# Optimization experiments

Measured on AMD Instinct MI355X. Metric: run time of the kernel, lower is better.

The kernel has to match this reference:

```python
import jax, jax.numpy as jnp
import numpy as np
from jax import lax

N = 16384          # num_nodes (LSTM sequence length, batch=1)
AVG_DEG = 32
E_EDGES = N * AVG_DEG
FEAT = 512         # cmd_args.feat_dim (tag vocab)
EMB = 256          # embedding_size -> LSTM input = 2*EMB
H = 512            # LSTM hidden_size
MLP_H = 512        # cmd_args.hidden
C = 10             # cmd_args.num_class


def setup_inputs() -> dict:
    key = jax.random.key(0)
    ks = jax.random.split(key, 14)
    s = 1.0 / np.sqrt(H)
    u = lambda k, shape: jax.random.uniform(k, shape, jnp.float32, -s, s)
    return {
        "node_tags": jax.random.randint(ks[0], (N,), 0, FEAT),
        "neighbor_node_ids": jax.random.randint(ks[1], (E_EDGES,), 0, N),
        "neighbor_tag_ids": jax.random.randint(ks[2], (E_EDGES,), 0, FEAT),
        "label": jax.random.randint(ks[3], (1,), 0, C),
        "W_emb": u(ks[4], (FEAT, EMB)),
        "b_emb": u(ks[5], (EMB,)),
        "W_ih": u(ks[6], (4 * H, 2 * EMB)),  # torch LSTM gate order: i, f, g, o
        "W_hh": u(ks[7], (4 * H, H)),
        "b_lstm": u(ks[8], (4 * H,)),        # b_ih + b_hh folded together
        "W1": u(ks[9], (H, MLP_H)),
        "b1": u(ks[10], (MLP_H,)),
        "W2": u(ks[11], (MLP_H, C)),
        "b2": u(ks[12], (C,)),
    }


def reference(node_tags, neighbor_node_ids, neighbor_tag_ids, label,
              W_emb, b_emb, W_ih, W_hh, b_lstm, W1, b1, W2, b2):
    n = node_tags.shape[0]
    feat_dim = W_emb.shape[0]
    hid = W_hh.shape[1]

    # one-hot(node_tags) @ W_emb + b  ==  row-gather of W_emb
    node_emb = W_emb[node_tags] + b_emb                      # [N, EMB]

    # ragged neighbor-tag histogram via scatter-add (the Python double loop)
    hist = jnp.zeros((n, feat_dim), dtype=W_emb.dtype)
    hist = hist.at[neighbor_node_ids, neighbor_tag_ids].add(1.0)  # [N, FEAT]
    nb_emb = hist @ W_emb + b_emb                            # [N, EMB]

    x = jnp.concatenate([node_emb, nb_emb], axis=1)          # [N, 2*EMB]

    # single-layer LSTM, batch=1, seq_len=N; precompute input projections
    pre = x @ W_ih.T + b_lstm                                # [N, 4H]

    def step(carry, p):
        h, c = carry
        g = p + h @ W_hh.T                                   # [4H]
        i, f, gg, o = jnp.split(g, 4)
        i = jax.nn.sigmoid(i)
        f = jax.nn.sigmoid(f)
        o = jax.nn.sigmoid(o)
        c = f * c + i * jnp.tanh(gg)
        h = o * jnp.tanh(c)
        return (h, c), h

    init = (jnp.zeros((hid,), x.dtype), jnp.zeros((hid,), x.dtype))
    _, hs = lax.scan(step, init, pre)                        # hs: [N, H]

    embed = jnp.sum(hs, axis=0)[None, :]                     # [1, H] (sum over time)

    # MLPClassifier: Linear -> ReLU -> Linear -> log_softmax
    h1 = jax.nn.relu(embed @ W1 + b1)
    logits = h1 @ W2 + b2                                    # [1, C]
    return jax.nn.log_softmax(logits, axis=-1)
```

## Files before the change

### kernel.cpp

```cpp
#include <hip/hip_runtime.h>
#include <hip/hip_bf16.h>

#define N_NODES 16384
#define E_EDGESN (16384*32)
#define FEAT 512
#define EMB 256
#define HID 512
#define G4 2048
#define XDIM 512
#define NWG 16
#define UPW 32

typedef __attribute__((ext_vector_type(8))) short bf16x8;
typedef __attribute__((ext_vector_type(4))) float f32x4;

__device__ __forceinline__ float b2f(unsigned short u) {
  union { unsigned int i; float f; } v; v.i = ((unsigned int)u) << 16; return v.f;
}
__device__ __forceinline__ unsigned short f2b(float f) {
  union { float f; unsigned int i; } v; v.f = f;
  unsigned int x = v.i;
  unsigned int r = (x + 0x7FFFu + ((x >> 16) & 1u)) >> 16;
  return (unsigned short)r;
}
__device__ __forceinline__ float sigmoidf_(float x) { return 1.0f / (1.0f + __expf(-x)); }

__global__ __launch_bounds__(256) void k_detect(const unsigned* __restrict__ w,
                                                unsigned* __restrict__ flag) {
  __shared__ int cnt;
  if (threadIdx.x == 0) cnt = 0;
  __syncthreads();
  int hits = 0;
#pragma unroll
  for (int j = 0; j < 4; ++j) {
    unsigned wv = w[threadIdx.x * 4 + j];
    unsigned e = (wv >> 7) & 0xFFu;
    if ((e >= 90u && e <= 126u) || ((wv & 0xFFFFu) == 0u)) hits++;
  }
  atomicAdd(&cnt, hits);
  __syncthreads();
  if (threadIdx.x == 0) *flag = (cnt < 512) ? 1u : 0u;
}

__global__ void k_convert(const void* __restrict__ src, unsigned short* __restrict__ dst,
                          int n, const unsigned* __restrict__ flag) {
  int i = blockIdx.x * blockDim.x + threadIdx.x;
  if (i >= n) return;
  if (*flag) dst[i] = f2b(((const float*)src)[i]);
  else       dst[i] = ((const unsigned short*)src)[i];
}

__global__ void k_hist(const int* __restrict__ nid, const int* __restrict__ ntag,
                       unsigned* __restrict__ hist) {
  int e = blockIdx.x * blockDim.x + threadIdx.x;
  if (e < E_EDGESN)
    atomicAdd(&hist[(size_t)nid[e] * FEAT + ntag[e]], 1u);
}

__global__ __launch_bounds__(256) void k_build_x(
    const int* __restrict__ tags, const unsigned* __restrict__ hist,
    const unsigned short* __restrict__ Wemb, const unsigned short* __restrict__ bemb,
    unsigned short* __restrict__ x) {
  __shared__ int f_lds[160];
  __shared__ float c_lds[160];
  __shared__ int nlist;
  int n = blockIdx.x, c = threadIdx.x;
  if (c == 0) nlist = 0;
  __syncthreads();
  for (int f = c; f < FEAT; f += 256) {
    unsigned cnt = hist[(size_t)n * FEAT + f];
    if (cnt) {
      int idx = atomicAdd(&nlist, 1);
      if (idx < 160) { f_lds[idx] = f; c_lds[idx] = (float)cnt; }
    }
  }
  __syncthreads();
  int m = nlist; if (m > 160) m = 160;
  float be = b2f(bemb[c]);
  int tg = tags[n];
  x[(size_t)n * XDIM + c] = f2b(b2f(Wemb[(size_t)tg * EMB + c]) + be);
  float acc = be;
  for (int j = 0; j < m; ++j)
    acc += c_lds[j] * b2f(Wemb[(size_t)f_lds[j] * EMB + c]);
  x[(size_t)n * XDIM + EMB + c] = f2b(acc);
}

__global__ __launch_bounds__(256) void k_gemm_pre(
    const unsigned short* __restrict__ x, const unsigned short* __restrict__ Wih,
    const unsigned short* __restrict__ blstm, unsigned short* __restrict__ pre) {
  int wave = threadIdx.x >> 6, lane = threadIdx.x & 63;
  int row = lane & 15, quad = lane >> 4;
  int mband = blockIdx.y * 64 + wave * 16;
  int nbase = blockIdx.x * 128;
  f32x4 acc[8] = {};
  const unsigned short* ap = x + (size_t)(mband + row) * XDIM + quad * 8;
  const unsigned short* bp0 = Wih + (size_t)(nbase + row) * XDIM + quad * 8;
  for (int kc = 0; kc < 16; ++kc) {
    bf16x8 af = *(const bf16x8*)(ap + kc * 32);
#pragma unroll
    for (int nt = 0; nt < 8; ++nt) {
      bf16x8 bf = *(const bf16x8*)(bp0 + (size_t)nt * 16 * XDIM + kc * 32);
      acc[nt] = __builtin_amdgcn_mfma_f32_16x16x32_bf16(af, bf, acc[nt], 0, 0, 0);
    }
  }
#pragma unroll
  for (int nt = 0; nt < 8; ++nt) {
    int nn = nbase + nt * 16 + row;
    float bv = b2f(blstm[nn]);
#pragma unroll
    for (int i = 0; i < 4; ++i) {
      int mm = mband + quad * 4 + i;
      pre[(size_t)mm * G4 + nn] = f2b(acc[nt][i] + bv);
    }
  }
}

__global__ __launch_bounds__(512, 2) void k_scan(
    const unsigned short* __restrict__ Whh, const unsigned short* __restrict__ pre,
    unsigned* __restrict__ hw, float* __restrict__ embed) {
  __shared__ float h_lds[HID];
  __shared__ float g_lds[128];
  int tid = threadIdx.x, wg = blockIdx.x;
  int rg = tid >> 4, s = tid & 15;

  int growA[4];
  float wreg[4][32];
#pragma unroll
  for (int rr = 0; rr < 4; ++rr) {
    int r = rg * 4 + rr;
    int grow = (r >> 5) * HID + wg * UPW + (r & 31);
    growA[rr] = grow;
    const unsigned short* wp = Whh + (size_t)grow * HID;
#pragma unroll
    for (int j = 0; j < 16; ++j) {
      wreg[rr][2 * j]     = b2f(wp[32 * j + 2 * s]);
      wreg[rr][2 * j + 1] = b2f(wp[32 * j + 2 * s + 1]);
    }
  }

  float pcur[4];
#pragma unroll
  for (int rr = 0; rr < 4; ++rr) pcur[rr] = b2f(pre[growA[rr]]);

  h_lds[tid] = 0.0f;
  float cstate = 0.0f, eacc = 0.0f;
  __syncthreads();

  for (int t = 0; t < N_NODES; ++t) {
    float a0 = 0.f, a1 = 0.f, a2 = 0.f, a3 = 0.f;
    const float2* hb = (const float2*)h_lds;
#pragma unroll
    for (int j = 0; j < 16; ++j) {
      float2 hv = hb[j * 16 + s];
      a0 += wreg[0][2*j] * hv.x + wreg[0][2*j+1] * hv.y;
      a1 += wreg[1][2*j] * hv.x + wreg[1][2*j+1] * hv.y;
      a2 += wreg[2][2*j] * hv.x + wreg[2][2*j+1] * hv.y;
      a3 += wreg[3][2*j] * hv.x + wreg[3][2*j+1] * hv.y;
    }
#pragma unroll
    for (int off = 1; off < 16; off <<= 1) {
      a0 += __shfl_xor(a0, off);
      a1 += __shfl_xor(a1, off);
      a2 += __shfl_xor(a2, off);
      a3 += __shfl_xor(a3, off);
    }
    if (s == 0) {
      g_lds[rg * 4 + 0] = a0 + pcur[0];
      g_lds[rg * 4 + 1] = a1 + pcur[1];
      g_lds[rg * 4 + 2] = a2 + pcur[2];
      g_lds[rg * 4 + 3] = a3 + pcur[3];
    }
    __syncthreads();

    unsigned tagw = (unsigned)t & 0xFFFFu;
    unsigned base = ((unsigned)t & 1u) * 1024u;
    if (tid < UPW) {
      float gi = sigmoidf_(g_lds[tid]);
      float gf = sigmoidf_(g_lds[32 + tid]);
      float gg = tanhf(g_lds[64 + tid]);
      float go = sigmoidf_(g_lds[96 + tid]);
      cstate = gf * cstate + gi * gg;
      float hn = go * tanhf(cstate);
      eacc += hn;
      union { float f; unsigned u; } cu; cu.f = hn;
      __hip_atomic_store(&hw[base + wg * UPW + tid], (cu.u & 0xFFFF0000u) | tagw,
                         __ATOMIC_RELAXED, __HIP_MEMORY_SCOPE_AGENT);
      __hip_atomic_store(&hw[base + 512 + wg * UPW + tid], (cu.u << 16) | tagw,
                         __ATOMIC_RELAXED, __HIP_MEMORY_SCOPE_AGENT);
    }
    if (s == 0 && (t + 1) < N_NODES) {
#pragma unroll
      for (int rr = 0; rr < 4; ++rr)
        pcur[rr] = b2f(pre[(size_t)(t + 1) * G4 + growA[rr]]);
    }
    if (t < N_NODES - 1) {
      unsigned v0, v1;
      for (;;) {
        v0 = __hip_atomic_load(&hw[base + tid],       __ATOMIC_RELAXED, __HIP_MEMORY_SCOPE_AGENT);
        v1 = __hip_atomic_load(&hw[base + 512 + tid], __ATOMIC_RELAXED, __HIP_MEMORY_SCOPE_AGENT);
        if ((((v0 ^ tagw) | (v1 ^ tagw)) & 0xFFFFu) == 0u) break;
        __builtin_amdgcn_s_sleep(1);
      }
      union { unsigned u; float f; } rc; rc.u = (v0 & 0xFFFF0000u) | (v1 >> 16);
      h_lds[tid] = rc.f;
      __syncthreads();
    }
  }
  if (tid < UPW) embed[wg * UPW + tid] = eacc;
}

__global__ __launch_bounds__(512) void k_head(
    const float* __restrict__ embed, const unsigned short* __restrict__ W1,
    const unsigned short* __restrict__ b1, const unsigned short* __restrict__ W2,
    const unsigned short* __restrict__ b2, void* __restrict__ out,
    const unsigned* __restrict__ flag) {
  __shared__ float e_s[HID], h1_s[HID];
  __shared__ float lg[16];
  int tid = threadIdx.x;
  e_s[tid] = embed[tid];
  __syncthreads();
  float sum = b2f(b1[tid]);
  for (int i = 0; i < HID; ++i)
    sum += e_s[i] * b2f(W1[(size_t)i * HID + tid]);
  h1_s[tid] = fmaxf(sum, 0.0f);
  __syncthreads();
  if (tid < 10) {
    float l = b2f(b2[tid]);
    for (int j = 0; j < HID; ++j)
      l += h1_s[j] * b2f(W2[(size_t)j * 10 + tid]);
    lg[tid] = l;
  }
  __syncthreads();
  if (tid == 0) {
    float m = -1e30f;
    for (int c = 0; c < 10; ++c) m = fmaxf(m, lg[c]);
    float se = 0.f;
    for (int c = 0; c < 10; ++c) se += expf(lg[c] - m);
    float lse = m + logf(se);
    if (*flag) {
      for (int c = 0; c < 10; ++c) ((float*)out)[c] = lg[c] - lse;
    } else {
      for (int c = 0; c < 10; ++c) ((unsigned short*)out)[c] = f2b(lg[c] - lse);
    }
  }
}

extern "C" void kernel_launch(void* const* d_in, const int* in_sizes, int n_in,
                              void* d_out, int out_size, void* d_ws, size_t ws_size,
                              hipStream_t stream) {
  const int* node_tags = (const int*)d_in[0];
  const int* nid = (const int*)d_in[1];
  const int* ntag = (const int*)d_in[2];

  char* ws = (char*)d_ws;
  unsigned short* pre  = (unsigned short*)ws;
  unsigned short* x    = (unsigned short*)(ws + 67108864);
  unsigned*       hist = (unsigned*)(ws + 83886080);
  char* tail = ws + 117440512;
  unsigned* hw    = (unsigned*)tail;
  unsigned* flag  = (unsigned*)(tail + 8192);
  float*    embed = (float*)(tail + 8448);
  char* wc = ws + 117456896;
  unsigned short* Wemb_c  = (unsigned short*)(wc);
  unsigned short* bemb_c  = (unsigned short*)(wc + 262144);
  unsigned short* Wih_c   = (unsigned short*)(wc + 262656);
  unsigned short* Whh_c   = (unsigned short*)(wc + 2359808);
  unsigned short* blstm_c = (unsigned short*)(wc + 4456960);
  unsigned short* W1_c    = (unsigned short*)(wc + 4461056);
  unsigned short* b1_c    = (unsigned short*)(wc + 4985344);
  unsigned short* W2_c    = (unsigned short*)(wc + 4986368);
  unsigned short* b2_c    = (unsigned short*)(wc + 4996608);

  hipMemsetAsync(hist, 0, 33554432, stream);

  k_detect<<<1, 256, 0, stream>>>((const unsigned*)d_in[6], flag);

  struct { const void* s; unsigned short* d; int n; } cv[9] = {
    { d_in[4],  Wemb_c,  FEAT * EMB },
    { d_in[5],  bemb_c,  EMB },
    { d_in[6],  Wih_c,   G4 * XDIM },
    { d_in[7],  Whh_c,   G4 * HID },
    { d_in[8],  blstm_c, G4 },
    { d_in[9],  W1_c,    HID * HID },
    { d_in[10], b1_c,    HID },
    { d_in[11], W2_c,    HID * 10 },
    { d_in[12], b2_c,    10 },
  };
  for (int i = 0; i < 9; ++i)
    k_convert<<<(cv[i].n + 255) / 256, 256, 0, stream>>>(cv[i].s, cv[i].d, cv[i].n, flag);

  k_hist<<<E_EDGESN / 256, 256, 0, stream>>>(nid, ntag, hist);
  k_build_x<<<N_NODES, 256, 0, stream>>>(node_tags, hist, Wemb_c, bemb_c, x);
  k_gemm_pre<<<dim3(G4 / 128, N_NODES / 64), 256, 0, stream>>>(x, Wih_c, blstm_c, pre);
  k_scan<<<NWG, 512, 0, stream>>>(Whh_c, pre, hw, embed);
  k_head<<<1, 512, 0, stream>>>(embed, W1_c, b1_c, W2_c, b2_c, d_out, flag);
}
```

Before: 32.83 ms.

## Co-locate LSTM scan workgroups on one XCD and streamline per-step gate exchange

Launches extra scan workgroups and uses an atomic election on the hardware XCC ID so the 16 working groups all run on the same XCD, keeping the cross-workgroup hidden-state exchange within one L2. It reorders the precomputed gate layout so each hidden unit's four gates sit next to each other. This lets each 16-lane group finish its own cell update without the shared-memory gate step and its extra barrier. The h exchange uses 64-bit stores and polling loads with explicit cache bits, and the gate activations use rcp-based sigmoid and tanh approximations. The risks are slightly lower precision, reliance on the XCD hardware register and on enough workgroups landing on one XCD, and extra launched blocks that exit early.

Measured after the change: 33.33 ms. Within noise of the previous version (+1.5%).

```diff
diff --git a/kernel.cpp b/kernel.cpp
--- a/kernel.cpp
+++ b/kernel.cpp
@@ -9,6 +9,7 @@
 #define G4 2048
 #define XDIM 512
 #define NWG 16
+#define NLAUNCH 128
 #define UPW 32
 
 typedef __attribute__((ext_vector_type(8))) short bf16x8;
@@ -23,7 +24,12 @@
   unsigned int r = (x + 0x7FFFu + ((x >> 16) & 1u)) >> 16;
   return (unsigned short)r;
 }
-__device__ __forceinline__ float sigmoidf_(float x) { return 1.0f / (1.0f + __expf(-x)); }
+__device__ __forceinline__ float fast_sigmoid(float x) {
+  return __builtin_amdgcn_rcpf(1.0f + __expf(-x));
+}
+__device__ __forceinline__ float fast_tanh(float x) {
+  return fmaf(-2.0f, __builtin_amdgcn_rcpf(1.0f + __expf(2.0f * x)), 1.0f);
+}
 
 __global__ __launch_bounds__(256) void k_detect(const unsigned* __restrict__ w,
                                                 unsigned* __restrict__ flag) {
@@ -107,44 +113,64 @@
   for (int nt = 0; nt < 8; ++nt) {
     int nn = nbase + nt * 16 + row;
     float bv = b2f(blstm[nn]);
+    int pn = ((nn & 511) << 2) | (nn >> 9);
 #pragma unroll
     for (int i = 0; i < 4; ++i) {
       int mm = mband + quad * 4 + i;
-      pre[(size_t)mm * G4 + nn] = f2b(acc[nt][i] + bv);
+      pre[(size_t)mm * G4 + pn] = f2b(acc[nt][i] + bv);
     }
   }
 }
 
 __global__ __launch_bounds__(512, 2) void k_scan(
-    const unsigned short* __restrict__ Whh, const unsigned short* __restrict__ pre,
-    unsigned* __restrict__ hw, float* __restrict__ embed) {
+    const unsigned short* __restrict__ Whh, const unsigned short* __restrict__ prep,
+    unsigned* __restrict__ hw, float* __restrict__ embed, int* __restrict__ elect) {
   __shared__ float h_lds[HID];
-  __shared__ float g_lds[128];
-  int tid = threadIdx.x, wg = blockIdx.x;
-  int rg = tid >> 4, s = tid & 15;
-
-  int growA[4];
+  __shared__ int rank_s;
+  int tid = threadIdx.x;
+
+  if (tid == 0) {
+    unsigned xcd;
+    asm volatile("s_getreg_b32 %0, hwreg(HW_REG_XCC_ID)" : "=s"(xcd));
+    xcd &= 7u;
+    int idx = atomicAdd(&elect[xcd], 1);
+    int rank = -1;
+    if (idx < NWG) {
+      if (idx == NWG - 1) atomicCAS(&elect[8], -1, (int)xcd);
+      int w;
+      while ((w = __hip_atomic_load(&elect[8], __ATOMIC_RELAXED,
+                                    __HIP_MEMORY_SCOPE_AGENT)) == -1)
+        __builtin_amdgcn_s_sleep(8);
+      if (w == (int)xcd) rank = idx;
+    }
+    rank_s = rank;
+  }
+  __syncthreads();
+  int wg = rank_s;
+  if (wg < 0) return;
+
+  int ug = tid >> 4;
+  int s  = tid & 15;
+  int unit = wg * UPW + ug;
+
   float wreg[4][32];
 #pragma unroll
-  for (int rr = 0; rr < 4; ++rr) {
-    int r = rg * 4 + rr;
-    int grow = (r >> 5) * HID + wg * UPW + (r & 31);
-    growA[rr] = grow;
-    const unsigned short* wp = Whh + (size_t)grow * HID;
+  for (int g = 0; g < 4; ++g) {
+    const unsigned short* wp = Whh + (size_t)(g * HID + unit) * HID;
 #pragma unroll
     for (int j = 0; j < 16; ++j) {
-      wreg[rr][2 * j]     = b2f(wp[32 * j + 2 * s]);
-      wreg[rr][2 * j + 1] = b2f(wp[32 * j + 2 * s + 1]);
-    }
-  }
-
-  float pcur[4];
-#pragma unroll
-  for (int rr = 0; rr < 4; ++rr) pcur[rr] = b2f(pre[growA[rr]]);
-
+      wreg[g][2 * j]     = b2f(wp[32 * j + 2 * s]);
+      wreg[g][2 * j + 1] = b2f(wp[32 * j + 2 * s + 1]);
+    }
+  }
+
+  ushort4 pc = *(const ushort4*)(prep + (size_t)unit * 4);
+  float cstate = 0.0f, eacc = 0.0f;
   h_lds[tid] = 0.0f;
-  float cstate = 0.0f, eacc = 0.0f;
-  __syncthreads();
+  __syncthreads();
+
+  unsigned long long hwB = (unsigned long long)hw;
+  int pollslow = 0;
 
   for (int t = 0; t < N_NODES; ++t) {
     float a0 = 0.f, a1 = 0.f, a2 = 0.f, a3 = 0.f;
@@ -164,49 +190,57 @@
       a2 += __shfl_xor(a2, off);
       a3 += __shfl_xor(a3, off);
     }
+
+    unsigned tagw = (unsigned)t;
+    unsigned long long sbase = hwB + (unsigned)((t & 1) << 12);
+
     if (s == 0) {
-      g_lds[rg * 4 + 0] = a0 + pcur[0];
-      g_lds[rg * 4 + 1] = a1 + pcur[1];
-      g_lds[rg * 4 + 2] = a2 + pcur[2];
-      g_lds[rg * 4 + 3] = a3 + pcur[3];
-    }
-    __syncthreads();
-
-    unsigned tagw = (unsigned)t & 0xFFFFu;
-    unsigned base = ((unsigned)t & 1u) * 1024u;
-    if (tid < UPW) {
-      float gi = sigmoidf_(g_lds[tid]);
-      float gf = sigmoidf_(g_lds[32 + tid]);
-      float gg = tanhf(g_lds[64 + tid]);
-      float go = sigmoidf_(g_lds[96 + tid]);
+      float gi = fast_sigmoid(a0 + b2f(pc.x));
+      float gf = fast_sigmoid(a1 + b2f(pc.y));
+      float gg = fast_tanh   (a2 + b2f(pc.z));
+      float go = fast_sigmoid(a3 + b2f(pc.w));
       cstate = gf * cstate + gi * gg;
-      float hn = go * tanhf(cstate);
+      float hn = go * fast_tanh(cstate);
       eacc += hn;
-      union { float f; unsigned u; } cu; cu.f = hn;
-      __hip_atomic_store(&hw[base + wg * UPW + tid], (cu.u & 0xFFFF0000u) | tagw,
-                         __ATOMIC_RELAXED, __HIP_MEMORY_SCOPE_AGENT);
-      __hip_atomic_store(&hw[base + 512 + wg * UPW + tid], (cu.u << 16) | tagw,
-                         __ATOMIC_RELAXED, __HIP_MEMORY_SCOPE_AGENT);
-    }
-    if (s == 0 && (t + 1) < N_NODES) {
-#pragma unroll
-      for (int rr = 0; rr < 4; ++rr)
-        pcur[rr] = b2f(pre[(size_t)(t + 1) * G4 + growA[rr]]);
-    }
+      if (t < N_NODES - 1) {
+        union { float f; unsigned u; } cu; cu.f = hn;
+        unsigned long long sv =
+            ((unsigned long long)((cu.u << 16) | tagw) << 32) |
+            (unsigned long long)((cu.u & 0xFFFF0000u) | tagw);
+        unsigned long long sa = sbase + 8u * (unsigned)unit;
+        asm volatile("global_store_dwordx2 %0, %1, off sc0 sc1"
+                     :: "v"(sa), "v"(sv) : "memory");
+      }
+    }
+    if (s == 0 && (t + 1) < N_NODES)
+      pc = *(const ushort4*)(prep + (size_t)(t + 1) * G4 + unit * 4);
+
     if (t < N_NODES - 1) {
+      unsigned long long pa = sbase + 8u * (unsigned)tid;
+      unsigned long long v64;
       unsigned v0, v1;
+      int spins = 0;
       for (;;) {
-        v0 = __hip_atomic_load(&hw[base + tid],       __ATOMIC_RELAXED, __HIP_MEMORY_SCOPE_AGENT);
-        v1 = __hip_atomic_load(&hw[base + 512 + tid], __ATOMIC_RELAXED, __HIP_MEMORY_SCOPE_AGENT);
-        if ((((v0 ^ tagw) | (v1 ^ tagw)) & 0xFFFFu) == 0u) break;
-        __builtin_amdgcn_s_sleep(1);
+        if (!pollslow) {
+          asm volatile("global_load_dwordx2 %0, %1, off sc0\n\ts_waitcnt vmcnt(0)"
+                       : "=v"(v64) : "v"(pa) : "memory");
+          v0 = (unsigned)v64; v1 = (unsigned)(v64 >> 32);
+          if ((((v0 ^ tagw) | (v1 ^ tagw)) & 0xFFFFu) == 0u) break;
+          if (++spins > 4096) pollslow = 1;
+        } else {
+          unsigned* pp = (unsigned*)(uintptr_t)pa;
+          v0 = __hip_atomic_load(pp,     __ATOMIC_RELAXED, __HIP_MEMORY_SCOPE_AGENT);
+          v1 = __hip_atomic_load(pp + 1, __ATOMIC_RELAXED, __HIP_MEMORY_SCOPE_AGENT);
+          if ((((v0 ^ tagw) | (v1 ^ tagw)) & 0xFFFFu) == 0u) break;
+          __builtin_amdgcn_s_sleep(1);
+        }
       }
       union { unsigned u; float f; } rc; rc.u = (v0 & 0xFFFF0000u) | (v1 >> 16);
       h_lds[tid] = rc.f;
       __syncthreads();
     }
   }
-  if (tid < UPW) embed[wg * UPW + tid] = eacc;
+  if (s == 0) embed[unit] = eacc;
 }
 
 __global__ __launch_bounds__(512) void k_head(
@@ -260,6 +294,7 @@
   unsigned* hw    = (unsigned*)tail;
   unsigned* flag  = (unsigned*)(tail + 8192);
   float*    embed = (float*)(tail + 8448);
+  int*      elect = (int*)(tail + 10496);
   char* wc = ws + 117456896;
   unsigned short* Wemb_c  = (unsigned short*)(wc);
   unsigned short* bemb_c  = (unsigned short*)(wc + 262144);
@@ -272,6 +307,8 @@
   unsigned short* b2_c    = (unsigned short*)(wc + 4996608);
 
   hipMemsetAsync(hist, 0, 33554432, stream);
+  hipMemsetAsync(elect, 0, 32, stream);
+  hipMemsetAsync(elect + 8, 0xFF, 4, stream);
 
   k_detect<<<1, 256, 0, stream>>>((const unsigned*)d_in[6], flag);
 
@@ -292,6 +329,6 @@
   k_hist<<<E_EDGESN / 256, 256, 0, stream>>>(nid, ntag, hist);
   k_build_x<<<N_NODES, 256, 0, stream>>>(node_tags, hist, Wemb_c, bemb_c, x);
   k_gemm_pre<<<dim3(G4 / 128, N_NODES / 64), 256, 0, stream>>>(x, Wih_c, blstm_c, pre);
-  k_scan<<<NWG, 512, 0, stream>>>(Whh_c, pre, hw, embed);
+  k_scan<<<NLAUNCH, 512, 0, stream>>>(Whh_c, pre, hw, embed, elect);
   k_head<<<1, 512, 0, stream>>>(embed, W1_c, b1_c, W2_c, b2_c, d_out, flag);
 }
```

## Restructure LSTM scan: per-unit gate ownership, direct global h reads, interleaved pre layout

Applied to the files above, without the earlier changes.

The recurrent scan now runs across 32 workgroups of 256 threads. Each 16-lane group owns all four gates of one hidden unit, so there is no LDS gate exchange or block barrier. The hidden state is published as one tagged 32-bit word per unit, with an 8-bit step tag packed into the low mantissa bits. Each lane reads its slice of h directly from global memory with cache-bypassing batched loads and checks the tags, which replaces the LDS staging and __syncthreads. The pre-activation GEMM writes gates interleaved per unit, so each unit's four gates come from two dwords prefetched eight steps ahead. Sigmoid and tanh use rcp-based fast approximations. The cost is reduced h precision (24-bit float, 8-bit tag), a shorter tag that wraps sooner, and more polling traffic per lane.

New measurement: 86.79 ms. +164.3%, slower.

```diff
diff --git a/kernel.cpp b/kernel.cpp
--- a/kernel.cpp
+++ b/kernel.cpp
@@ -8,8 +8,8 @@
 #define HID 512
 #define G4 2048
 #define XDIM 512
-#define NWG 16
-#define UPW 32
+#define NWG 32
+#define UPW 16
 
 typedef __attribute__((ext_vector_type(8))) short bf16x8;
 typedef __attribute__((ext_vector_type(4))) float f32x4;
@@ -23,7 +23,12 @@
   unsigned int r = (x + 0x7FFFu + ((x >> 16) & 1u)) >> 16;
   return (unsigned short)r;
 }
-__device__ __forceinline__ float sigmoidf_(float x) { return 1.0f / (1.0f + __expf(-x)); }
+__device__ __forceinline__ float fast_sigmoid(float x) {
+  return __builtin_amdgcn_rcpf(1.0f + __expf(-x));
+}
+__device__ __forceinline__ float fast_tanh(float x) {
+  return fmaf(-2.0f, __builtin_amdgcn_rcpf(1.0f + __expf(2.0f * x)), 1.0f);
+}
 
 __global__ __launch_bounds__(256) void k_detect(const unsigned* __restrict__ w,
                                                 unsigned* __restrict__ flag) {
@@ -107,55 +112,124 @@
   for (int nt = 0; nt < 8; ++nt) {
     int nn = nbase + nt * 16 + row;
     float bv = b2f(blstm[nn]);
+    int pn = ((nn & 511) << 2) | (nn >> 9);
 #pragma unroll
     for (int i = 0; i < 4; ++i) {
       int mm = mband + quad * 4 + i;
-      pre[(size_t)mm * G4 + nn] = f2b(acc[nt][i] + bv);
-    }
-  }
-}
-
-__global__ __launch_bounds__(512, 2) void k_scan(
-    const unsigned short* __restrict__ Whh, const unsigned short* __restrict__ pre,
+      pre[(size_t)mm * G4 + pn] = f2b(acc[nt][i] + bv);
+    }
+  }
+}
+
+__global__ __launch_bounds__(256, 1) void k_scan(
+    const unsigned short* __restrict__ Whh, const unsigned short* __restrict__ prep,
     unsigned* __restrict__ hw, float* __restrict__ embed) {
-  __shared__ float h_lds[HID];
-  __shared__ float g_lds[128];
   int tid = threadIdx.x, wg = blockIdx.x;
-  int rg = tid >> 4, s = tid & 15;
-
-  int growA[4];
+  int ug = tid >> 4;
+  int s  = tid & 15;
+  int lane = tid & 63;
+  int unit = wg * UPW + ug;
+
   float wreg[4][32];
 #pragma unroll
-  for (int rr = 0; rr < 4; ++rr) {
-    int r = rg * 4 + rr;
-    int grow = (r >> 5) * HID + wg * UPW + (r & 31);
-    growA[rr] = grow;
-    const unsigned short* wp = Whh + (size_t)grow * HID;
+  for (int g = 0; g < 4; ++g) {
+    const unsigned* wp = (const unsigned*)(Whh + (size_t)(g * HID + unit) * HID) + s * 16;
 #pragma unroll
     for (int j = 0; j < 16; ++j) {
-      wreg[rr][2 * j]     = b2f(wp[32 * j + 2 * s]);
-      wreg[rr][2 * j + 1] = b2f(wp[32 * j + 2 * s + 1]);
-    }
-  }
-
-  float pcur[4];
-#pragma unroll
-  for (int rr = 0; rr < 4; ++rr) pcur[rr] = b2f(pre[growA[rr]]);
-
-  h_lds[tid] = 0.0f;
+      unsigned wv = wp[j];
+      wreg[g][2 * j]     = b2f((unsigned short)(wv & 0xFFFFu));
+      wreg[g][2 * j + 1] = b2f((unsigned short)(wv >> 16));
+    }
+  }
+
+  unsigned pc0[8], pc1[8];
+  if (s == 1) {
+#pragma unroll
+    for (int i = 0; i < 8; ++i) {
+      const unsigned* pp = (const unsigned*)(prep + (size_t)i * G4 + (unsigned)unit * 4u);
+      pc0[i] = pp[0]; pc1[i] = pp[1];
+    }
+  }
+  int bsrc = (lane & 48) | 1;
+
   float cstate = 0.0f, eacc = 0.0f;
-  __syncthreads();
+  unsigned long long hwB = (unsigned long long)hw;
+  unsigned w32[32];
+#pragma unroll
+  for (int i = 0; i < 32; ++i) w32[i] = 0;
 
   for (int t = 0; t < N_NODES; ++t) {
+    if (t > 0) {
+      unsigned tagp = (unsigned)(t - 1) & 0xFFu;
+      unsigned long long pa = hwB + (unsigned)(((t - 1) & 1) << 11) + (unsigned)s * 128u;
+      unsigned long long r0,r1,r2,r3,r4,r5,r6,r7,r8,r9,r10,r11,r12,r13,r14,r15;
+      int ok = 0;
+      for (int tries = 0; tries < 64 && !ok; ++tries) {
+        asm volatile(
+          "global_load_dwordx2 %0, %16, off sc0 sc1\n\t"
+          "global_load_dwordx2 %1, %16, off offset:8 sc0 sc1\n\t"
+          "global_load_dwordx2 %2, %16, off offset:16 sc0 sc1\n\t"
+          "global_load_dwordx2 %3, %16, off offset:24 sc0 sc1\n\t"
+          "global_load_dwordx2 %4, %16, off offset:32 sc0 sc1\n\t"
+          "global_load_dwordx2 %5, %16, off offset:40 sc0 sc1\n\t"
+          "global_load_dwordx2 %6, %16, off offset:48 sc0 sc1\n\t"
+          "global_load_dwordx2 %7, %16, off offset:56 sc0 sc1\n\t"
+          "global_load_dwordx2 %8, %16, off offset:64 sc0 sc1\n\t"
+          "global_load_dwordx2 %9, %16, off offset:72 sc0 sc1\n\t"
+          "global_load_dwordx2 %10, %16, off offset:80 sc0 sc1\n\t"
+          "global_load_dwordx2 %11, %16, off offset:88 sc0 sc1\n\t"
+          "global_load_dwordx2 %12, %16, off offset:96 sc0 sc1\n\t"
+          "global_load_dwordx2 %13, %16, off offset:104 sc0 sc1\n\t"
+          "global_load_dwordx2 %14, %16, off offset:112 sc0 sc1\n\t"
+          "global_load_dwordx2 %15, %16, off offset:120 sc0 sc1\n\t"
+          "s_waitcnt vmcnt(0)"
+          : "=&v"(r0), "=&v"(r1), "=&v"(r2), "=&v"(r3),
+            "=&v"(r4), "=&v"(r5), "=&v"(r6), "=&v"(r7),
+            "=&v"(r8), "=&v"(r9), "=&v"(r10), "=&v"(r11),
+            "=&v"(r12), "=&v"(r13), "=&v"(r14), "=&v"(r15)
+          : "v"(pa) : "memory");
+        w32[0]=(unsigned)r0;  w32[1]=(unsigned)(r0>>32);
+        w32[2]=(unsigned)r1;  w32[3]=(unsigned)(r1>>32);
+        w32[4]=(unsigned)r2;  w32[5]=(unsigned)(r2>>32);
+        w32[6]=(unsigned)r3;  w32[7]=(unsigned)(r3>>32);
+        w32[8]=(unsigned)r4;  w32[9]=(unsigned)(r4>>32);
+        w32[10]=(unsigned)r5; w32[11]=(unsigned)(r5>>32);
+        w32[12]=(unsigned)r6; w32[13]=(unsigned)(r6>>32);
+        w32[14]=(unsigned)r7; w32[15]=(unsigned)(r7>>32);
+        w32[16]=(unsigned)r8; w32[17]=(unsigned)(r8>>32);
+        w32[18]=(unsigned)r9; w32[19]=(unsigned)(r9>>32);
+        w32[20]=(unsigned)r10; w32[21]=(unsigned)(r10>>32);
+        w32[22]=(unsigned)r11; w32[23]=(unsigned)(r11>>32);
+        w32[24]=(unsigned)r12; w32[25]=(unsigned)(r12>>32);
+        w32[26]=(unsigned)r13; w32[27]=(unsigned)(r13>>32);
+        w32[28]=(unsigned)r14; w32[29]=(unsigned)(r14>>32);
+        w32[30]=(unsigned)r15; w32[31]=(unsigned)(r15>>32);
+        unsigned m = 0;
+#pragma unroll
+        for (int i = 0; i < 32; ++i) m |= (w32[i] ^ tagp);
+        ok = ((m & 0xFFu) == 0u);
+      }
+      if (!ok) {
+        unsigned* qp = (unsigned*)(uintptr_t)pa;
+#pragma unroll
+        for (int i = 0; i < 32; ++i) {
+          unsigned v;
+          do {
+            v = __hip_atomic_load(qp + i, __ATOMIC_RELAXED, __HIP_MEMORY_SCOPE_AGENT);
+          } while (((v ^ tagp) & 0xFFu) != 0u);
+          w32[i] = v;
+        }
+      }
+    }
+
     float a0 = 0.f, a1 = 0.f, a2 = 0.f, a3 = 0.f;
-    const float2* hb = (const float2*)h_lds;
-#pragma unroll
-    for (int j = 0; j < 16; ++j) {
-      float2 hv = hb[j * 16 + s];
-      a0 += wreg[0][2*j] * hv.x + wreg[0][2*j+1] * hv.y;
-      a1 += wreg[1][2*j] * hv.x + wreg[1][2*j+1] * hv.y;
-      a2 += wreg[2][2*j] * hv.x + wreg[2][2*j+1] * hv.y;
-      a3 += wreg[3][2*j] * hv.x + wreg[3][2*j+1] * hv.y;
+#pragma unroll
+    for (int j = 0; j < 32; ++j) {
+      union { unsigned u; float f; } hv; hv.u = w32[j] & 0xFFFFFF00u;
+      a0 = fmaf(wreg[0][j], hv.f, a0);
+      a1 = fmaf(wreg[1][j], hv.f, a1);
+      a2 = fmaf(wreg[2][j], hv.f, a2);
+      a3 = fmaf(wreg[3][j], hv.f, a3);
     }
 #pragma unroll
     for (int off = 1; off < 16; off <<= 1) {
@@ -164,49 +238,37 @@
       a2 += __shfl_xor(a2, off);
       a3 += __shfl_xor(a3, off);
     }
+
+    unsigned w0 = __shfl(pc0[t & 7], bsrc, 64);
+    unsigned w1 = __shfl(pc1[t & 7], bsrc, 64);
+
     if (s == 0) {
-      g_lds[rg * 4 + 0] = a0 + pcur[0];
-      g_lds[rg * 4 + 1] = a1 + pcur[1];
-      g_lds[rg * 4 + 2] = a2 + pcur[2];
-      g_lds[rg * 4 + 3] = a3 + pcur[3];
-    }
-    __syncthreads();
-
-    unsigned tagw = (unsigned)t & 0xFFFFu;
-    unsigned base = ((unsigned)t & 1u) * 1024u;
-    if (tid < UPW) {
-      float gi = sigmoidf_(g_lds[tid]);
-      float gf = sigmoidf_(g_lds[32 + tid]);
-      float gg = tanhf(g_lds[64 + tid]);
-      float go = sigmoidf_(g_lds[96 + tid]);
+      float gi = fast_sigmoid(a0 + b2f((unsigned short)(w0 & 0xFFFFu)));
+      float gf = fast_sigmoid(a1 + b2f((unsigned short)(w0 >> 16)));
+      float gg = fast_tanh   (a2 + b2f((unsigned short)(w1 & 0xFFFFu)));
+      float go = fast_sigmoid(a3 + b2f((unsigned short)(w1 >> 16)));
       cstate = gf * cstate + gi * gg;
-      float hn = go * tanhf(cstate);
+      float hn = go * fast_tanh(cstate);
       eacc += hn;
-      union { float f; unsigned u; } cu; cu.f = hn;
-      __hip_atomic_store(&hw[base + wg * UPW + tid], (cu.u & 0xFFFF0000u) | tagw,
-                         __ATOMIC_RELAXED, __HIP_MEMORY_SCOPE_AGENT);
-      __hip_atomic_store(&hw[base + 512 + wg * UPW + tid], (cu.u << 16) | tagw,
-                         __ATOMIC_RELAXED, __HIP_MEMORY_SCOPE_AGENT);
-    }
-    if (s == 0 && (t + 1) < N_NODES) {
-#pragma unroll
-      for (int rr = 0; rr < 4; ++rr)
-        pcur[rr] = b2f(pre[(size_t)(t + 1) * G4 + growA[rr]]);
-    }
-    if (t < N_NODES - 1) {
-      unsigned v0, v1;
-      for (;;) {
-        v0 = __hip_atomic_load(&hw[base + tid],       __ATOMIC_RELAXED, __HIP_MEMORY_SCOPE_AGENT);
-        v1 = __hip_atomic_load(&hw[base + 512 + tid], __ATOMIC_RELAXED, __HIP_MEMORY_SCOPE_AGENT);
-        if ((((v0 ^ tagw) | (v1 ^ tagw)) & 0xFFFFu) == 0u) break;
-        __builtin_amdgcn_s_sleep(1);
+      if (t < N_NODES - 1) {
+        union { float f; unsigned u; } cu; cu.f = hn;
+        unsigned word = (cu.u & 0xFFFFFF00u) | ((unsigned)t & 0xFFu);
+        unsigned long long sa = hwB + (unsigned)((t & 1) << 11) + (unsigned)unit * 4u;
+        asm volatile("global_store_dword %0, %1, off sc0 sc1"
+                     :: "v"(sa), "v"(word) : "memory");
       }
-      union { unsigned u; float f; } rc; rc.u = (v0 & 0xFFFF0000u) | (v1 >> 16);
-      h_lds[tid] = rc.f;
-      __syncthreads();
-    }
-  }
-  if (tid < UPW) embed[wg * UPW + tid] = eacc;
+    }
+    if (s == 1 && (t & 7) == 7) {
+#pragma unroll
+      for (int i = 0; i < 8; ++i) {
+        int row = t + 1 + i;
+        if (row >= N_NODES) row = 0;
+        const unsigned* pp = (const unsigned*)(prep + (size_t)row * G4 + (unsigned)unit * 4u);
+        pc0[i] = pp[0]; pc1[i] = pp[1];
+      }
+    }
+  }
+  if (s == 0) embed[unit] = eacc;
 }
 
 __global__ __launch_bounds__(512) void k_head(
@@ -258,9 +320,9 @@
   unsigned*       hist = (unsigned*)(ws + 83886080);
   char* tail = ws + 117440512;
   unsigned* hw    = (unsigned*)tail;
-  unsigned* flag  = (unsigned*)(tail + 8192);
-  float*    embed = (float*)(tail + 8448);
-  char* wc = ws + 117456896;
+  unsigned* flag  = (unsigned*)(tail + 4096);
+  float*    embed = (float*)(tail + 4352);
+  char* wc = tail + 8192;
   unsigned short* Wemb_c  = (unsigned short*)(wc);
   unsigned short* bemb_c  = (unsigned short*)(wc + 262144);
   unsigned short* Wih_c   = (unsigned short*)(wc + 262656);
@@ -292,6 +354,6 @@
   k_hist<<<E_EDGESN / 256, 256, 0, stream>>>(nid, ntag, hist);
   k_build_x<<<N_NODES, 256, 0, stream>>>(node_tags, hist, Wemb_c, bemb_c, x);
   k_gemm_pre<<<dim3(G4 / 128, N_NODES / 64), 256, 0, stream>>>(x, Wih_c, blstm_c, pre);
-  k_scan<<<NWG, 512, 0, stream>>>(Whh_c, pre, hw, embed);
+  k_scan<<<NWG, 256, 0, stream>>>(Whh_c, pre, hw, embed);
   k_head<<<1, 512, 0, stream>>>(embed, W1_c, b1_c, W2_c, b2_c, d_out, flag);
 }
```

## Restructure LSTM scan: 32 workgroups, in-register gates, replicated h exchange

Applied to the files above, without the earlier changes.

Splits the recurrent scan across 32 workgroups of 256 threads, each thread group owning one hidden unit with all four gate rows. This removes the intermediate gate LDS buffer and one barrier per step. The pre-activation matrix is permuted so each unit's four gates sit together and are prefetched eight steps at a time into registers. Hidden state is exchanged as fp32 with an 8-bit tag (previously split into bf16 halves) through four replicated global buffers, read with 64-bit loads and spin-polled with fewer sleeps. Fast rcp-based sigmoid and tanh are used, and truncating the mantissa to carry the tag slightly changes precision.

Measured after the change: 29.88 ms. 9.0% less time.

```diff
diff --git a/kernel.cpp b/kernel.cpp
--- a/kernel.cpp
+++ b/kernel.cpp
@@ -8,8 +8,10 @@
 #define HID 512
 #define G4 2048
 #define XDIM 512
-#define NWG 16
-#define UPW 32
+#define NWG 32
+#define UPW 16
+#define NREP 4
+#define REPW 4096
 
 typedef __attribute__((ext_vector_type(8))) short bf16x8;
 typedef __attribute__((ext_vector_type(4))) float f32x4;
@@ -23,7 +25,12 @@
   unsigned int r = (x + 0x7FFFu + ((x >> 16) & 1u)) >> 16;
   return (unsigned short)r;
 }
-__device__ __forceinline__ float sigmoidf_(float x) { return 1.0f / (1.0f + __expf(-x)); }
+__device__ __forceinline__ float fast_sigmoid(float x) {
+  return __builtin_amdgcn_rcpf(1.0f + __expf(-x));
+}
+__device__ __forceinline__ float fast_tanh(float x) {
+  return fmaf(-2.0f, __builtin_amdgcn_rcpf(1.0f + __expf(2.0f * x)), 1.0f);
+}
 
 __global__ __launch_bounds__(256) void k_detect(const unsigned* __restrict__ w,
                                                 unsigned* __restrict__ flag) {
@@ -107,44 +114,53 @@
   for (int nt = 0; nt < 8; ++nt) {
     int nn = nbase + nt * 16 + row;
     float bv = b2f(blstm[nn]);
+    int pn = ((nn & 511) << 2) | (nn >> 9);
 #pragma unroll
     for (int i = 0; i < 4; ++i) {
       int mm = mband + quad * 4 + i;
-      pre[(size_t)mm * G4 + nn] = f2b(acc[nt][i] + bv);
-    }
-  }
-}
-
-__global__ __launch_bounds__(512, 2) void k_scan(
-    const unsigned short* __restrict__ Whh, const unsigned short* __restrict__ pre,
+      pre[(size_t)mm * G4 + pn] = f2b(acc[nt][i] + bv);
+    }
+  }
+}
+
+__global__ __launch_bounds__(256, 1) void k_scan(
+    const unsigned short* __restrict__ Whh, const unsigned short* __restrict__ prep,
     unsigned* __restrict__ hw, float* __restrict__ embed) {
   __shared__ float h_lds[HID];
-  __shared__ float g_lds[128];
   int tid = threadIdx.x, wg = blockIdx.x;
-  int rg = tid >> 4, s = tid & 15;
-
-  int growA[4];
+  int ug = tid >> 4;
+  int s  = tid & 15;
+  int lane = tid & 63;
+  int unit = wg * UPW + ug;
+
   float wreg[4][32];
 #pragma unroll
-  for (int rr = 0; rr < 4; ++rr) {
-    int r = rg * 4 + rr;
-    int grow = (r >> 5) * HID + wg * UPW + (r & 31);
-    growA[rr] = grow;
-    const unsigned short* wp = Whh + (size_t)grow * HID;
+  for (int g = 0; g < 4; ++g) {
+    const unsigned* wp = (const unsigned*)(Whh + (size_t)(g * HID + unit) * HID);
 #pragma unroll
     for (int j = 0; j < 16; ++j) {
-      wreg[rr][2 * j]     = b2f(wp[32 * j + 2 * s]);
-      wreg[rr][2 * j + 1] = b2f(wp[32 * j + 2 * s + 1]);
-    }
-  }
-
-  float pcur[4];
-#pragma unroll
-  for (int rr = 0; rr < 4; ++rr) pcur[rr] = b2f(pre[growA[rr]]);
-
+      unsigned wv = wp[16 * j + s];
+      wreg[g][2 * j]     = b2f((unsigned short)(wv & 0xFFFFu));
+      wreg[g][2 * j + 1] = b2f((unsigned short)(wv >> 16));
+    }
+  }
+
+  unsigned pc0[8], pc1[8];
+  if (s == 4) {
+#pragma unroll
+    for (int i = 0; i < 8; ++i) {
+      const unsigned* pp = (const unsigned*)(prep + (size_t)i * G4 + (unsigned)unit * 4u);
+      pc0[i] = pp[0]; pc1[i] = pp[1];
+    }
+  }
+  int bsrc = (lane & 48) | 4;
+
+  float cstate = 0.0f, eacc = 0.0f;
   h_lds[tid] = 0.0f;
-  float cstate = 0.0f, eacc = 0.0f;
-  __syncthreads();
+  h_lds[256 + tid] = 0.0f;
+  __syncthreads();
+
+  unsigned myrep = (unsigned)(wg & (NREP - 1));
 
   for (int t = 0; t < N_NODES; ++t) {
     float a0 = 0.f, a1 = 0.f, a2 = 0.f, a3 = 0.f;
@@ -164,49 +180,63 @@
       a2 += __shfl_xor(a2, off);
       a3 += __shfl_xor(a3, off);
     }
-    if (s == 0) {
-      g_lds[rg * 4 + 0] = a0 + pcur[0];
-      g_lds[rg * 4 + 1] = a1 + pcur[1];
-      g_lds[rg * 4 + 2] = a2 + pcur[2];
-      g_lds[rg * 4 + 3] = a3 + pcur[3];
-    }
-    __syncthreads();
-
-    unsigned tagw = (unsigned)t & 0xFFFFu;
-    unsigned base = ((unsigned)t & 1u) * 1024u;
-    if (tid < UPW) {
-      float gi = sigmoidf_(g_lds[tid]);
-      float gf = sigmoidf_(g_lds[32 + tid]);
-      float gg = tanhf(g_lds[64 + tid]);
-      float go = sigmoidf_(g_lds[96 + tid]);
-      cstate = gf * cstate + gi * gg;
-      float hn = go * tanhf(cstate);
-      eacc += hn;
+
+    unsigned w0 = __shfl(pc0[t & 7], bsrc, 64);
+    unsigned w1 = __shfl(pc1[t & 7], bsrc, 64);
+
+    float gi = fast_sigmoid(a0 + b2f((unsigned short)(w0 & 0xFFFFu)));
+    float gf = fast_sigmoid(a1 + b2f((unsigned short)(w0 >> 16)));
+    float gg = fast_tanh   (a2 + b2f((unsigned short)(w1 & 0xFFFFu)));
+    float go = fast_sigmoid(a3 + b2f((unsigned short)(w1 >> 16)));
+    cstate = gf * cstate + gi * gg;
+    float hn = go * fast_tanh(cstate);
+    if (s == 0) eacc += hn;
+
+    unsigned tagw = (unsigned)t & 0xFFu;
+    if (t < N_NODES - 1) {
       union { float f; unsigned u; } cu; cu.f = hn;
-      __hip_atomic_store(&hw[base + wg * UPW + tid], (cu.u & 0xFFFF0000u) | tagw,
-                         __ATOMIC_RELAXED, __HIP_MEMORY_SCOPE_AGENT);
-      __hip_atomic_store(&hw[base + 512 + wg * UPW + tid], (cu.u << 16) | tagw,
-                         __ATOMIC_RELAXED, __HIP_MEMORY_SCOPE_AGENT);
-    }
-    if (s == 0 && (t + 1) < N_NODES) {
-#pragma unroll
-      for (int rr = 0; rr < 4; ++rr)
-        pcur[rr] = b2f(pre[(size_t)(t + 1) * G4 + growA[rr]]);
-    }
+      unsigned word = (cu.u & 0xFFFFFF00u) | tagw;
+      unsigned slotw = ((unsigned)t & 1u) << 9;
+      if (s == 0) {
+        __hip_atomic_store(&hw[0 * REPW + slotw + unit], word,
+                           __ATOMIC_RELAXED, __HIP_MEMORY_SCOPE_AGENT);
+        __hip_atomic_store(&hw[1 * REPW + slotw + unit], word,
+                           __ATOMIC_RELAXED, __HIP_MEMORY_SCOPE_AGENT);
+      } else if (s == 8) {
+        __hip_atomic_store(&hw[2 * REPW + slotw + unit], word,
+                           __ATOMIC_RELAXED, __HIP_MEMORY_SCOPE_AGENT);
+        __hip_atomic_store(&hw[3 * REPW + slotw + unit], word,
+                           __ATOMIC_RELAXED, __HIP_MEMORY_SCOPE_AGENT);
+      }
+    }
+    if (s == 4 && (t & 7) == 7) {
+#pragma unroll
+      for (int i = 0; i < 8; ++i) {
+        int row = t + 1 + i;
+        if (row >= N_NODES) row = 0;
+        const unsigned* pp = (const unsigned*)(prep + (size_t)row * G4 + (unsigned)unit * 4u);
+        pc0[i] = pp[0]; pc1[i] = pp[1];
+      }
+    }
+
     if (t < N_NODES - 1) {
+      unsigned long long* qp = (unsigned long long*)
+          (hw + myrep * REPW + (((unsigned)t & 1u) << 9)) + tid;
       unsigned v0, v1;
+      int tries = 0;
       for (;;) {
-        v0 = __hip_atomic_load(&hw[base + tid],       __ATOMIC_RELAXED, __HIP_MEMORY_SCOPE_AGENT);
-        v1 = __hip_atomic_load(&hw[base + 512 + tid], __ATOMIC_RELAXED, __HIP_MEMORY_SCOPE_AGENT);
-        if ((((v0 ^ tagw) | (v1 ^ tagw)) & 0xFFFFu) == 0u) break;
-        __builtin_amdgcn_s_sleep(1);
+        unsigned long long v = __hip_atomic_load(qp, __ATOMIC_RELAXED,
+                                                 __HIP_MEMORY_SCOPE_AGENT);
+        v0 = (unsigned)v; v1 = (unsigned)(v >> 32);
+        if ((((v0 ^ tagw) | (v1 ^ tagw)) & 0xFFu) == 0u) break;
+        if (++tries > 128) __builtin_amdgcn_s_sleep(1);
       }
-      union { unsigned u; float f; } rc; rc.u = (v0 & 0xFFFF0000u) | (v1 >> 16);
-      h_lds[tid] = rc.f;
+      h_lds[2 * tid]     = __uint_as_float(v0 & 0xFFFFFF00u);
+      h_lds[2 * tid + 1] = __uint_as_float(v1 & 0xFFFFFF00u);
       __syncthreads();
     }
   }
-  if (tid < UPW) embed[wg * UPW + tid] = eacc;
+  if (s == 0) embed[unit] = eacc;
 }
 
 __global__ __launch_bounds__(512) void k_head(
@@ -258,9 +288,9 @@
   unsigned*       hist = (unsigned*)(ws + 83886080);
   char* tail = ws + 117440512;
   unsigned* hw    = (unsigned*)tail;
-  unsigned* flag  = (unsigned*)(tail + 8192);
-  float*    embed = (float*)(tail + 8448);
-  char* wc = ws + 117456896;
+  unsigned* flag  = (unsigned*)(tail + 65536);
+  float*    embed = (float*)(tail + 65792);
+  char* wc = tail + 69632;
   unsigned short* Wemb_c  = (unsigned short*)(wc);
   unsigned short* bemb_c  = (unsigned short*)(wc + 262144);
   unsigned short* Wih_c   = (unsigned short*)(wc + 262656);
@@ -292,6 +322,6 @@
   k_hist<<<E_EDGESN / 256, 256, 0, stream>>>(nid, ntag, hist);
   k_build_x<<<N_NODES, 256, 0, stream>>>(node_tags, hist, Wemb_c, bemb_c, x);
   k_gemm_pre<<<dim3(G4 / 128, N_NODES / 64), 256, 0, stream>>>(x, Wih_c, blstm_c, pre);
-  k_scan<<<NWG, 512, 0, stream>>>(Whh_c, pre, hw, embed);
+  k_scan<<<NWG, 256, 0, stream>>>(Whh_c, pre, hw, embed);
   k_head<<<1, 512, 0, stream>>>(embed, W1_c, b1_c, W2_c, b2_c, d_out, flag);
 }
```
